# Kernel optimization log

Measured on AMD Instinct MI355X. Metric: run time of the kernel, lower is better.

The kernel has to match this reference:

```python
import jax, jax.numpy as jnp
import numpy as np

D_MODEL, D_K, D_V = 512, 64, 64
B, S = 8, 4096


def setup_inputs() -> dict:
    key = jax.random.key(0)
    ks = jax.random.split(key, 10)
    scale = 1.0 / np.sqrt(D_MODEL)
    return {
        "q": jax.random.normal(ks[0], (B, S, D_MODEL), dtype=jnp.float32),
        "k": jax.random.normal(ks[1], (B, S, D_MODEL), dtype=jnp.float32),
        "v": jax.random.normal(ks[2], (B, S, D_MODEL), dtype=jnp.float32),
        "mask": jax.random.randint(ks[3], (B, S), 0, 2, dtype=jnp.int32),
        "Wq": jax.random.uniform(ks[4], (D_MODEL, D_K), jnp.float32, -scale, scale),
        "bq": jax.random.uniform(ks[5], (D_K,), jnp.float32, -scale, scale),
        "Wk": jax.random.uniform(ks[6], (D_MODEL, D_K), jnp.float32, -scale, scale),
        "bk": jax.random.uniform(ks[7], (D_K,), jnp.float32, -scale, scale),
        "Wv": jax.random.uniform(ks[8], (D_MODEL, D_V), jnp.float32, -scale, scale),
        "bv": jax.random.uniform(ks[9], (D_V,), jnp.float32, -scale, scale),
    }


def reference(q, k, v, mask, Wq, bq, Wk, bk, Wv, bv):
    # single-head QKV projections
    qh = jnp.einsum("bsd,dk->bsk", q, Wq) + bq  # [B,S,d_k]
    kh = jnp.einsum("bsd,dk->bsk", k, Wk) + bk  # [B,S,d_k]
    vh = jnp.einsum("bsd,dv->bsv", v, Wv) + bv  # [B,S,d_v]
    scores = jnp.einsum("bqk,bsk->bqs", qh, kh) / jnp.sqrt(jnp.float32(D_K))
    # key-padding mask: mask [B,S] -> [B,1,S], masked positions -> -1e10
    scores = jnp.where(mask[:, None, :] == 0, jnp.float32(-1e10), scores)
    attn = jax.nn.softmax(scores, axis=-1)
    return jnp.einsum("bqs,bsv->bqv", attn, vh)
```

## Files before the change

kernel.cpp:

```cpp
#include <hip/hip_runtime.h>

typedef __attribute__((ext_vector_type(8))) short bf16x8;
typedef __attribute__((ext_vector_type(4))) float f32x4;
typedef __attribute__((ext_vector_type(4))) unsigned short u16x4;

__device__ __forceinline__ short f2bf(float f) {
  unsigned int u = __builtin_bit_cast(unsigned int, f);
  u += 0x7fffu + ((u >> 16) & 1u);
  return (short)(u >> 16);
}

__global__ void prep_w(const float* __restrict__ Wq, const float* __restrict__ Wk,
                       const float* __restrict__ Wv, unsigned short* __restrict__ wt) {
  int idx = blockIdx.x * 256 + threadIdx.x;
  int m = idx >> 15;
  int rem = idx & 32767;
  int n = rem >> 9;
  int k = rem & 511;
  const float* W = (m == 0) ? Wq : ((m == 1) ? Wk : Wv);
  wt[idx] = (unsigned short)f2bf(W[k * 64 + n]);
}

__global__ __launch_bounds__(256) void proj_kernel(
    const float* __restrict__ qx, const float* __restrict__ kx, const float* __restrict__ vx,
    const unsigned short* __restrict__ wt, const int* __restrict__ mask,
    const float* __restrict__ bqp, const float* __restrict__ bkp, const float* __restrict__ bvp,
    unsigned short* __restrict__ qo, unsigned short* __restrict__ ko,
    unsigned short* __restrict__ vo) {
  __shared__ unsigned short lds[64 * 256];
  const int mode = blockIdx.y;
  const float* x = (mode == 0) ? qx : ((mode == 1) ? kx : vx);
  const float* bias = (mode == 0) ? bqp : ((mode == 1) ? bkp : bvp);
  const unsigned short* wtm = wt + mode * (64 * 512);
  const float osc = (mode == 0) ? 0.18033688011112042f : 1.0f;

  const int tid = threadIdx.x;
  const int w = tid >> 6, lane = tid & 63;
  const int g = lane >> 4, ln = lane & 15;
  const int rowbase = blockIdx.x * 128;

  const f32x4 fz = {0.f, 0.f, 0.f, 0.f};
  f32x4 acc[2][4];
#pragma unroll
  for (int mi = 0; mi < 2; ++mi)
#pragma unroll
    for (int nf = 0; nf < 4; ++nf) acc[mi][nf] = fz;

  for (int half = 0; half < 2; ++half) {
    __syncthreads();
#pragma unroll
    for (int i = 0; i < 8; ++i) {
      int c = tid + i * 256;
      int n = c >> 5, kc = c & 31;
      bf16x8 d = *reinterpret_cast<const bf16x8*>(wtm + n * 512 + half * 256 + kc * 8);
      int bo = (n * 512 + kc * 16) ^ ((n & 7) << 4);
      *reinterpret_cast<bf16x8*>(reinterpret_cast<char*>(lds) + bo) = d;
    }
    __syncthreads();
#pragma unroll
    for (int ks = 0; ks < 8; ++ks) {
      bf16x8 afrag[2];
#pragma unroll
      for (int mi = 0; mi < 2; ++mi) {
        int row = rowbase + w * 32 + mi * 16 + ln;
        const float4* ap = reinterpret_cast<const float4*>(
            x + (size_t)row * 512 + half * 256 + ks * 32 + g * 8);
        float4 a0 = ap[0], a1 = ap[1];
        bf16x8 af;
        af[0] = f2bf(a0.x); af[1] = f2bf(a0.y); af[2] = f2bf(a0.z); af[3] = f2bf(a0.w);
        af[4] = f2bf(a1.x); af[5] = f2bf(a1.y); af[6] = f2bf(a1.z); af[7] = f2bf(a1.w);
        afrag[mi] = af;
      }
#pragma unroll
      for (int nf = 0; nf < 4; ++nf) {
        int n = nf * 16 + ln;
        int bo = (n * 512 + ks * 64 + g * 16) ^ ((n & 7) << 4);
        bf16x8 bfrag = *reinterpret_cast<const bf16x8*>(reinterpret_cast<const char*>(lds) + bo);
        acc[0][nf] = __builtin_amdgcn_mfma_f32_16x16x32_bf16(afrag[0], bfrag, acc[0][nf], 0, 0, 0);
        acc[1][nf] = __builtin_amdgcn_mfma_f32_16x16x32_bf16(afrag[1], bfrag, acc[1][nf], 0, 0, 0);
      }
    }
  }

  float bc[4];
#pragma unroll
  for (int nf = 0; nf < 4; ++nf) bc[nf] = bias[nf * 16 + ln];

  if (mode < 2) {
    unsigned short* o = (mode == 0) ? qo : ko;
#pragma unroll
    for (int mi = 0; mi < 2; ++mi)
#pragma unroll
      for (int nf = 0; nf < 4; ++nf)
#pragma unroll
        for (int r = 0; r < 4; ++r) {
          int row = rowbase + w * 32 + mi * 16 + g * 4 + r;
          o[(size_t)row * 64 + nf * 16 + ln] = (unsigned short)f2bf((acc[mi][nf][r] + bc[nf]) * osc);
        }
  } else {
    __syncthreads();
#pragma unroll
    for (int mi = 0; mi < 2; ++mi)
#pragma unroll
      for (int nf = 0; nf < 4; ++nf)
#pragma unroll
        for (int r = 0; r < 4; ++r) {
          int srow = w * 32 + mi * 16 + g * 4 + r;
          lds[srow * 64 + nf * 16 + ln] = (unsigned short)f2bf(acc[mi][nf][r] + bc[nf]);
        }
    __syncthreads();
    int b = rowbase >> 12, s0 = rowbase & 4095;
    int dv = tid & 63, sc = tid >> 6;
#pragma unroll
    for (int i = 0; i < 4; ++i) {
      int sbase = s0 + sc * 32 + i * 8;
      const int* mrow = mask + b * 4096 + sbase;
      bf16x8 pack;
#pragma unroll
      for (int j = 0; j < 8; ++j) {
        short vv = (short)lds[(sc * 32 + i * 8 + j) * 64 + dv];
        pack[j] = mrow[j] ? vv : (short)0;
      }
      *reinterpret_cast<bf16x8*>(vo + (size_t)(b * 64 + dv) * 4096 + sbase) = pack;
    }
  }
}

#define KVBLK 128
#define NTILES 32

__global__ __launch_bounds__(256) void attn_kernel(
    const unsigned short* __restrict__ qh, const unsigned short* __restrict__ kh,
    const unsigned short* __restrict__ vt, const int* __restrict__ mask,
    float* __restrict__ out) {
  __shared__ unsigned short kt[2][KVBLK * 64];
  __shared__ unsigned short vv[2][80 * 128];

  const int b = blockIdx.y;
  const int qbase = blockIdx.x * 128;
  const int tid = threadIdx.x;
  const int w = tid >> 6, lane = tid & 63;
  const int g = lane >> 4, ln = lane & 15;

  for (int i = tid; i < 15 * 128; i += 256) {
    vv[0][65 * 128 + i] = 0;
    vv[1][65 * 128 + i] = 0;
  }

  bf16x8 qa[2][2];
#pragma unroll
  for (int qf = 0; qf < 2; ++qf) {
    int row = qbase + w * 32 + qf * 16 + ln;
    const unsigned short* qp = qh + (size_t)(b * 4096 + row) * 64;
    qa[qf][0] = *reinterpret_cast<const bf16x8*>(qp + g * 8);
    qa[qf][1] = *reinterpret_cast<const bf16x8*>(qp + 32 + g * 8);
  }

  const f32x4 fz = {0.f, 0.f, 0.f, 0.f};
  f32x4 accO[2][5];
#pragma unroll
  for (int qf = 0; qf < 2; ++qf)
#pragma unroll
    for (int nf = 0; nf < 5; ++nf) accO[qf][nf] = fz;

  const unsigned short* khb = kh + (size_t)b * 4096 * 64;
  const unsigned short* vtb = vt + (size_t)b * 64 * 4096;

  bf16x8 kreg[4], vreg[4];
  int mreg = 0;
  auto issue = [&](int ti) {
    int kvbase = ti * KVBLK;
#pragma unroll
    for (int i = 0; i < 4; ++i) {
      int c = tid + i * 256;
      vreg[i] = *reinterpret_cast<const bf16x8*>(vtb + (size_t)(c >> 4) * 4096 + kvbase + (c & 15) * 8);
      kreg[i] = *reinterpret_cast<const bf16x8*>(khb + (size_t)(kvbase + (c >> 3)) * 64 + (c & 7) * 8);
    }
    if (tid < KVBLK) mreg = mask[b * 4096 + kvbase + tid];
  };
  auto commit = [&](int bs) {
#pragma unroll
    for (int i = 0; i < 4; ++i) {
      int c = tid + i * 256;
      int kbo = ((c >> 3) * 128 + (c & 7) * 16) ^ (((c >> 3) & 7) << 4);
      *reinterpret_cast<bf16x8*>(reinterpret_cast<char*>(kt[bs]) + kbo) = kreg[i];
      int dv = c >> 4;
      int P0 = (c & 15) * 8;
      int c2 = P0 >> 5, h = (P0 >> 4) & 1, gg = (P0 >> 2) & 3;
      int x1 = 32 * c2 + 8 * gg + 4 * h;
      int swz = (dv & 7) << 4;
      union { bf16x8 v; u16x4 h4[2]; } sp; sp.v = vreg[i];
      *reinterpret_cast<u16x4*>(reinterpret_cast<char*>(vv[bs]) + ((dv * 256 + 2 * x1) ^ swz)) = sp.h4[0];
      *reinterpret_cast<u16x4*>(reinterpret_cast<char*>(vv[bs]) + ((dv * 256 + 2 * x1 + 16) ^ swz)) = sp.h4[1];
    }
    if (tid < KVBLK) {
      int p = tid;
      int x = 32 * (p >> 5) + 8 * ((p >> 2) & 3) + 4 * ((p >> 4) & 1) + (p & 3);
      vv[bs][64 * 128 + x] = mreg ? (unsigned short)0x3F80 : (unsigned short)0;
    }
  };

  issue(0);
  commit(0);
  __syncthreads();
  int cur = 0;

  for (int ti = 0; ti < NTILES; ++ti) {
    if (ti + 1 < NTILES) issue(ti + 1);

    f32x4 s0[8], s1[8];
#pragma unroll
    for (int nf = 0; nf < 8; ++nf) { s0[nf] = fz; s1[nf] = fz; }
#pragma unroll
    for (int c2 = 0; c2 < 2; ++c2)
#pragma unroll
      for (int nf = 0; nf < 8; ++nf) {
        int kvr = nf * 16 + ln;
        int bo = (kvr * 128 + c2 * 64 + g * 16) ^ ((kvr & 7) << 4);
        bf16x8 kf = *reinterpret_cast<const bf16x8*>(reinterpret_cast<const char*>(kt[cur]) + bo);
        s0[nf] = __builtin_amdgcn_mfma_f32_16x16x32_bf16(kf, qa[0][c2], s0[nf], 0, 0, 0);
        s1[nf] = __builtin_amdgcn_mfma_f32_16x16x32_bf16(kf, qa[1][c2], s1[nf], 0, 0, 0);
      }

    unsigned int pw[2][4][4];
#pragma unroll
    for (int c2 = 0; c2 < 4; ++c2)
#pragma unroll
      for (int hh = 0; hh < 2; ++hh) {
        {
          float p0 = __builtin_exp2f(s0[2 * c2 + hh][0]);
          float p1 = __builtin_exp2f(s0[2 * c2 + hh][1]);
          float p2 = __builtin_exp2f(s0[2 * c2 + hh][2]);
          float p3 = __builtin_exp2f(s0[2 * c2 + hh][3]);
          unsigned int w0, w1;
          asm("v_cvt_pk_bf16_f32 %0, %1, %2" : "=v"(w0) : "v"(p0), "v"(p1));
          asm("v_cvt_pk_bf16_f32 %0, %1, %2" : "=v"(w1) : "v"(p2), "v"(p3));
          pw[0][c2][2 * hh] = w0;
          pw[0][c2][2 * hh + 1] = w1;
        }
        {
          float p0 = __builtin_exp2f(s1[2 * c2 + hh][0]);
          float p1 = __builtin_exp2f(s1[2 * c2 + hh][1]);
          float p2 = __builtin_exp2f(s1[2 * c2 + hh][2]);
          float p3 = __builtin_exp2f(s1[2 * c2 + hh][3]);
          unsigned int w0, w1;
          asm("v_cvt_pk_bf16_f32 %0, %1, %2" : "=v"(w0) : "v"(p0), "v"(p1));
          asm("v_cvt_pk_bf16_f32 %0, %1, %2" : "=v"(w1) : "v"(p2), "v"(p3));
          pw[1][c2][2 * hh] = w0;
          pw[1][c2][2 * hh + 1] = w1;
        }
      }

#pragma unroll
    for (int c2 = 0; c2 < 4; ++c2) {
      union { unsigned int u[4]; bf16x8 v; } pa0, pa1;
#pragma unroll
      for (int t = 0; t < 4; ++t) { pa0.u[t] = pw[0][c2][t]; pa1.u[t] = pw[1][c2][t]; }
#pragma unroll
      for (int nf = 0; nf < 5; ++nf) {
        int dvr = nf * 16 + ln;
        int bo = (dvr * 256 + c2 * 64 + g * 16) ^ ((dvr & 7) << 4);
        bf16x8 vb = *reinterpret_cast<const bf16x8*>(reinterpret_cast<const char*>(vv[cur]) + bo);
        accO[0][nf] = __builtin_amdgcn_mfma_f32_16x16x32_bf16(pa0.v, vb, accO[0][nf], 0, 0, 0);
        accO[1][nf] = __builtin_amdgcn_mfma_f32_16x16x32_bf16(pa1.v, vb, accO[1][nf], 0, 0, 0);
      }
    }

    if (ti + 1 < NTILES) commit(cur ^ 1);
    __syncthreads();
    cur ^= 1;
  }

#pragma unroll
  for (int qf = 0; qf < 2; ++qf)
#pragma unroll
    for (int r = 0; r < 4; ++r) {
      float lv = __shfl(accO[qf][4][r], lane & 48);
      float rv = __builtin_amdgcn_rcpf(lv);
      int row = qbase + w * 32 + qf * 16 + g * 4 + r;
#pragma unroll
      for (int nf = 0; nf < 4; ++nf)
        out[(size_t)(b * 4096 + row) * 64 + nf * 16 + ln] = accO[qf][nf][r] * rv;
    }
}

extern "C" void kernel_launch(void* const* d_in, const int* in_sizes, int n_in,
                              void* d_out, int out_size, void* d_ws, size_t ws_size,
                              hipStream_t stream) {
  const float* q = (const float*)d_in[0];
  const float* k = (const float*)d_in[1];
  const float* v = (const float*)d_in[2];
  const int* mask = (const int*)d_in[3];
  const float* Wq = (const float*)d_in[4];
  const float* bq = (const float*)d_in[5];
  const float* Wk = (const float*)d_in[6];
  const float* bk = (const float*)d_in[7];
  const float* Wv = (const float*)d_in[8];
  const float* bv = (const float*)d_in[9];

  unsigned short* wsu = (unsigned short*)d_ws;
  unsigned short* qh = wsu;
  unsigned short* kh = qh + 2097152;
  unsigned short* vt = kh + 2097152;
  unsigned short* wt = vt + 2097152;

  prep_w<<<384, 256, 0, stream>>>(Wq, Wk, Wv, wt);
  proj_kernel<<<dim3(256, 3), 256, 0, stream>>>(q, k, v, wt, mask, bq, bk, bv, qh, kh, vt);
  attn_kernel<<<dim3(32, 8), 256, 0, stream>>>(qh, kh, vt, mask, (float*)d_out);
}
```

Baseline: 120.7 us.

## Split attention over KV halves with a combine kernel and MFMA priority hints

Splits the KV sequence into two halves across a new grid dimension, doubling the number of attention workgroups from 256 to 512. Each half writes unnormalized partial outputs and row sums, and a new combine kernel adds them and normalizes. This targets under-occupancy on a GPU with many CUs, and also raises the scheduling priority around the MFMA sections. The cost is an extra kernel launch plus writing and reading partial outputs through global memory. Skipping max subtraction works here only because the scores stay bounded.

```diff
diff --git a/kernel.cpp b/kernel.cpp
--- a/kernel.cpp
+++ b/kernel.cpp
@@ -127,16 +127,21 @@
 }
 
 #define KVBLK 128
-#define NTILES 32
-
-__global__ __launch_bounds__(256) void attn_kernel(
+#define NT 16
+
+__global__ __launch_bounds__(256, 2) void attn_kernel(
     const unsigned short* __restrict__ qh, const unsigned short* __restrict__ kh,
     const unsigned short* __restrict__ vt, const int* __restrict__ mask,
-    float* __restrict__ out) {
+    float* __restrict__ out0, float* __restrict__ out1,
+    float* __restrict__ l0p, float* __restrict__ l1p) {
   __shared__ unsigned short kt[2][KVBLK * 64];
   __shared__ unsigned short vv[2][80 * 128];
 
   const int b = blockIdx.y;
+  const int z = blockIdx.z;
+  const int kv0 = z * (NT * KVBLK);
+  float* __restrict__ optr = z ? out1 : out0;
+  float* __restrict__ lptr = z ? l1p : l0p;
   const int qbase = blockIdx.x * 128;
   const int tid = threadIdx.x;
   const int w = tid >> 6, lane = tid & 63;
@@ -169,7 +174,7 @@
   bf16x8 kreg[4], vreg[4];
   int mreg = 0;
   auto issue = [&](int ti) {
-    int kvbase = ti * KVBLK;
+    int kvbase = kv0 + ti * KVBLK;
 #pragma unroll
     for (int i = 0; i < 4; ++i) {
       int c = tid + i * 256;
@@ -205,12 +210,13 @@
   __syncthreads();
   int cur = 0;
 
-  for (int ti = 0; ti < NTILES; ++ti) {
-    if (ti + 1 < NTILES) issue(ti + 1);
+  for (int ti = 0; ti < NT; ++ti) {
+    if (ti + 1 < NT) issue(ti + 1);
 
     f32x4 s0[8], s1[8];
 #pragma unroll
     for (int nf = 0; nf < 8; ++nf) { s0[nf] = fz; s1[nf] = fz; }
+    __builtin_amdgcn_s_setprio(1);
 #pragma unroll
     for (int c2 = 0; c2 < 2; ++c2)
 #pragma unroll
@@ -221,6 +227,7 @@
         s0[nf] = __builtin_amdgcn_mfma_f32_16x16x32_bf16(kf, qa[0][c2], s0[nf], 0, 0, 0);
         s1[nf] = __builtin_amdgcn_mfma_f32_16x16x32_bf16(kf, qa[1][c2], s1[nf], 0, 0, 0);
       }
+    __builtin_amdgcn_s_setprio(0);
 
     unsigned int pw[2][4][4];
 #pragma unroll
@@ -251,6 +258,7 @@
         }
       }
 
+    __builtin_amdgcn_s_setprio(1);
 #pragma unroll
     for (int c2 = 0; c2 < 4; ++c2) {
       union { unsigned int u[4]; bf16x8 v; } pa0, pa1;
@@ -265,8 +273,9 @@
         accO[1][nf] = __builtin_amdgcn_mfma_f32_16x16x32_bf16(pa1.v, vb, accO[1][nf], 0, 0, 0);
       }
     }
-
-    if (ti + 1 < NTILES) commit(cur ^ 1);
+    __builtin_amdgcn_s_setprio(0);
+
+    if (ti + 1 < NT) commit(cur ^ 1);
     __syncthreads();
     cur ^= 1;
   }
@@ -275,13 +284,27 @@
   for (int qf = 0; qf < 2; ++qf)
 #pragma unroll
     for (int r = 0; r < 4; ++r) {
-      float lv = __shfl(accO[qf][4][r], lane & 48);
-      float rv = __builtin_amdgcn_rcpf(lv);
-      int row = qbase + w * 32 + qf * 16 + g * 4 + r;
+      int grow = b * 4096 + qbase + w * 32 + qf * 16 + g * 4 + r;
 #pragma unroll
       for (int nf = 0; nf < 4; ++nf)
-        out[(size_t)(b * 4096 + row) * 64 + nf * 16 + ln] = accO[qf][nf][r] * rv;
-    }
+        optr[(size_t)grow * 64 + nf * 16 + ln] = accO[qf][nf][r];
+      if (ln == 0) lptr[grow] = accO[qf][4][r];
+    }
+}
+
+__global__ __launch_bounds__(256) void combine_kernel(
+    float* __restrict__ out, const float* __restrict__ po1,
+    const float* __restrict__ l0p, const float* __restrict__ l1p) {
+  int idx = blockIdx.x * 256 + threadIdx.x;
+  int row = idx >> 4;
+  float rl = 1.0f / (l0p[row] + l1p[row]);
+  float4 a = reinterpret_cast<float4*>(out)[idx];
+  float4 c = reinterpret_cast<const float4*>(po1)[idx];
+  a.x = (a.x + c.x) * rl;
+  a.y = (a.y + c.y) * rl;
+  a.z = (a.z + c.z) * rl;
+  a.w = (a.w + c.w) * rl;
+  reinterpret_cast<float4*>(out)[idx] = a;
 }
 
 extern "C" void kernel_launch(void* const* d_in, const int* in_sizes, int n_in,
@@ -298,13 +321,18 @@
   const float* Wv = (const float*)d_in[8];
   const float* bv = (const float*)d_in[9];
 
-  unsigned short* wsu = (unsigned short*)d_ws;
-  unsigned short* qh = wsu;
-  unsigned short* kh = qh + 2097152;
-  unsigned short* vt = kh + 2097152;
-  unsigned short* wt = vt + 2097152;
+  char* wsb = (char*)d_ws;
+  unsigned short* qh = (unsigned short*)(wsb);
+  unsigned short* kh = (unsigned short*)(wsb + (4u << 20));
+  unsigned short* vt = (unsigned short*)(wsb + (8u << 20));
+  unsigned short* wt = (unsigned short*)(wsb + (12u << 20));
+  float* po1 = (float*)(wsb + (12u << 20) + 196608);
+  float* l0p = (float*)(wsb + (12u << 20) + 196608 + (8u << 20));
+  float* l1p = l0p + 32768;
 
   prep_w<<<384, 256, 0, stream>>>(Wq, Wk, Wv, wt);
   proj_kernel<<<dim3(256, 3), 256, 0, stream>>>(q, k, v, wt, mask, bq, bk, bv, qh, kh, vt);
-  attn_kernel<<<dim3(32, 8), 256, 0, stream>>>(qh, kh, vt, mask, (float*)d_out);
-}
+  attn_kernel<<<dim3(32, 8, 2), 256, 0, stream>>>(qh, kh, vt, mask,
+                                                  (float*)d_out, po1, l0p, l1p);
+  combine_kernel<<<2048, 256, 0, stream>>>((float*)d_out, po1, l0p, l1p);
+}
```

After: 111.8 us. 7.4% less time.
